# Optimization experiments

Measured on AMD Instinct MI355X. Metric: run time of the kernel, lower is better.

The kernel has to match this reference:

```python
import jax, jax.numpy as jnp
import numpy as np

DIM = 1024
NH = 16        # query heads
NKV = 4        # kv heads
HD = 64        # head dim
GROUPS = NH // NKV
SPATIAL = 16
NZ = SPATIAL * SPATIAL  # 256 latent tokens with 2D structure
SOFT_CAP = 50.0
SCALE = HD ** -0.5
EPS = 1e-6


def rope_2d_cos_sin(nz, hd, spatial, dtype):
    # 2D RoPE: first half of head_dim encodes row position, second half column.
    pos = jnp.arange(nz)
    row = (pos // spatial).astype(jnp.float32)
    col = (pos % spatial).astype(jnp.float32)
    quarter = hd // 4
    inv_freq = 1.0 / (10000.0 ** (jnp.arange(quarter, dtype=jnp.float32) / quarter))
    f_row = row[:, None] * inv_freq[None, :]   # (nz, hd/4)
    f_col = col[:, None] * inv_freq[None, :]   # (nz, hd/4)
    emb = jnp.concatenate([f_row, f_col], axis=-1)      # (nz, hd/2)
    emb = jnp.concatenate([emb, emb], axis=-1)          # (nz, hd)
    return jnp.cos(emb).astype(dtype), jnp.sin(emb).astype(dtype)


def rotate_half(x):
    x1, x2 = jnp.split(x, 2, axis=-1)
    return jnp.concatenate([-x2, x1], axis=-1)


def apply_rotary(x, cos, sin):
    return x * cos + rotate_half(x) * sin


def rms_norm(x, w):
    # RMSNorm over head_dim with learned per-dim scale (QKNorm)
    return x * jax.lax.rsqrt(jnp.mean(x * x, axis=-1, keepdims=True) + EPS) * w


def setup_inputs() -> dict:
    key = jax.random.key(0)
    ks = jax.random.split(key, 7)
    B, T, S = 4, 16, 264
    x = jax.random.normal(ks[0], (B, T, S, DIM), dtype=jnp.float32)
    wq = jax.random.normal(ks[1], (NH * HD, DIM), dtype=jnp.float32) * 0.02
    wk = jax.random.normal(ks[2], (NKV * HD, DIM), dtype=jnp.float32) * 0.02
    wv = jax.random.normal(ks[3], (NKV * HD, DIM), dtype=jnp.float32) * 0.02
    wo = jax.random.normal(ks[4], (DIM, NH * HD), dtype=jnp.float32) * 0.02
    q_norm_w = jnp.ones((HD,), dtype=jnp.float32)
    k_norm_w = jnp.ones((HD,), dtype=jnp.float32)
    return {"x": x, "wq": wq, "wk": wk, "wv": wv, "wo": wo,
            "q_norm_w": q_norm_w, "k_norm_w": k_norm_w}


def reference(x, wq, wk, wv, wo, q_norm_w, k_norm_w):
    B, T, S, D = x.shape
    xf = x.reshape(B * T, S, D)
    # projections (torch Linear: y = x @ W.T)
    q = (xf @ wq.T).reshape(B * T, S, NH, HD).transpose(0, 2, 1, 3)   # (BT,NH,S,HD)
    k = (xf @ wk.T).reshape(B * T, S, NKV, HD).transpose(0, 2, 1, 3)  # (BT,NKV,S,HD)
    v = (xf @ wv.T).reshape(B * T, S, NKV, HD).transpose(0, 2, 1, 3)
    # QKNorm
    q = rms_norm(q, q_norm_w)
    k = rms_norm(k, k_norm_w)
    # partial 2D RoPE on latent tokens only
    cos, sin = rope_2d_cos_sin(NZ, HD, SPATIAL, q.dtype)
    cos = cos[None, None]  # (1,1,NZ,HD)
    sin = sin[None, None]
    q = jnp.concatenate([apply_rotary(q[:, :, :NZ], cos, sin), q[:, :, NZ:]], axis=2)
    k = jnp.concatenate([apply_rotary(k[:, :, :NZ], cos, sin), k[:, :, NZ:]], axis=2)
    # GQA: expand kv heads (repeat_interleave == jnp.repeat)
    k = jnp.repeat(k, GROUPS, axis=1)
    v = jnp.repeat(v, GROUPS, axis=1)
    # attention with soft cap
    attn = jnp.einsum("bhqd,bhkd->bhqk", q, k) * SCALE
    attn = SOFT_CAP * jnp.tanh(attn / SOFT_CAP)
    attn = jax.nn.softmax(attn, axis=-1)
    out = jnp.einsum("bhqk,bhkd->bhqd", attn, v)
    out = out.transpose(0, 2, 1, 3).reshape(B * T, S, NH * HD)
    out = out @ wo.T
    return out.reshape(B, T, S, D)
```

## Files before the change

### kernel.cpp

```cpp
#include <hip/hip_runtime.h>

typedef __bf16 bf16;
typedef __bf16 bf16x8 __attribute__((ext_vector_type(8)));
typedef float  f32x4  __attribute__((ext_vector_type(4)));

#define DIM   1024
#define NH    16
#define NKV   4
#define HD    64
#define SLEN  264
#define BTOT  64
#define MROWS (BTOT * SLEN)
#define NQKV  1536
#define NZ    256
#define VPAD  288

__device__ __forceinline__ void gl_lds16(const bf16* g, bf16* l) {
    __builtin_amdgcn_global_load_lds((__attribute__((address_space(1))) void*)(g),
                                     (__attribute__((address_space(3))) void*)(l),
                                     16, 0, 0);
}

__global__ void cvt_f32_bf16(const float* __restrict__ src, bf16* __restrict__ dst, int n) {
    int i = (blockIdx.x * 256 + threadIdx.x) * 4;
    if (i < n) {
        float4 v = *(const float4*)(src + i);
        dst[i + 0] = (bf16)v.x; dst[i + 1] = (bf16)v.y;
        dst[i + 2] = (bf16)v.z; dst[i + 3] = (bf16)v.w;
    }
}

__global__ void cvt_wcat(const float* __restrict__ wq, const float* __restrict__ wk,
                         const float* __restrict__ wv, bf16* __restrict__ dst) {
    int i = (blockIdx.x * 256 + threadIdx.x) * 4;
    const float* src; int off;
    if (i < 1024 * 1024)      { src = wq; off = i; }
    else if (i < 1280 * 1024) { src = wk; off = i - 1024 * 1024; }
    else                      { src = wv; off = i - 1280 * 1024; }
    float4 v = *(const float4*)(src + off);
    dst[i + 0] = (bf16)v.x; dst[i + 1] = (bf16)v.y;
    dst[i + 2] = (bf16)v.z; dst[i + 3] = (bf16)v.w;
}

__global__ void rope_tab_kernel(float2* __restrict__ ctab) {
    int i = blockIdx.x * 256 + threadIdx.x;
    int s = i >> 5, d = i & 31;
    const float LN1 = 0.5756462732485115f;
    float pos = (d < 16) ? (float)(s >> 4) : (float)(s & 15);
    float ang = pos * expf(-(float)(d & 15) * LN1);
    float sn, cs; sincosf(ang, &sn, &cs);
    ctab[i] = make_float2(cs, sn);
}

__device__ __forceinline__ int xcd_swizzle(int orig, int nwg) {
    int q = nwg >> 3, r = nwg & 7;
    int xcd = orig & 7, lid = orig >> 3;
    return (xcd < r ? xcd * (q + 1) : r * (q + 1) + (xcd - r) * q) + lid;
}


#define GATE2  asm volatile("s_waitcnt vmcnt(2)" ::: "memory")
#define NOGATE do {} while (0)

#define STAGE(DST, G, H, KT) do {                                              \
    gl_lds16((G) + (size_t)((H) * 128 + rs0) * DIM + (KT) * 64 + cs0 * 8,      \
             (DST) + wid * 512);                                               \
    gl_lds16((G) + (size_t)((H) * 128 + 64 + rs0) * DIM + (KT) * 64 + cs0 * 8, \
             (DST) + 4096 + wid * 512);                                        \
} while (0)

#define PHASE(Ad, Bd, AA, KS, STAGE_STMT, GATE_STMT) do {                      \
    bf16x8 af_[4], bf_[4];                                                     \
    _Pragma("unroll")                                                          \
    for (int i_ = 0; i_ < 4; i_++) {                                           \
        af_[i_] = *(const bf16x8*)((Ad) + aRdBase + i_ * 1024 + xorv[KS]);     \
        bf_[i_] = *(const bf16x8*)((Bd) + bRdBase + i_ * 1024 + xorv[KS]);     \
    }                                                                          \
    STAGE_STMT;                                                                \
    GATE_STMT;                                                                 \
    __builtin_amdgcn_s_barrier();                                              \
    asm volatile("s_waitcnt lgkmcnt(0)" ::: "memory");                         \
    __builtin_amdgcn_sched_barrier(0);                                         \
    __builtin_amdgcn_s_setprio(1);                                             \
    _Pragma("unroll")                                                          \
    for (int i_ = 0; i_ < 4; i_++)                                             \
        _Pragma("unroll")                                                      \
        for (int n_ = 0; n_ < 4; n_++)                                         \
            acc[AA][i_][n_] = __builtin_amdgcn_mfma_f32_16x16x32_bf16(         \
                af_[i_], bf_[n_], acc[AA][i_][n_], 0, 0, 0);                   \
    __builtin_amdgcn_s_setprio(0);                                             \
    __builtin_amdgcn_s_barrier();                                              \
} while (0)

__device__ __forceinline__ void gemm256_core(const bf16* __restrict__ Ag,
                                             const bf16* __restrict__ Bg,
                                             f32x4 (&acc)[2][4][4]) {
    __shared__ __align__(16) bf16 A00[128 * 64], A01[128 * 64], A10[128 * 64], A11[128 * 64];
    __shared__ __align__(16) bf16 B00[128 * 64], B01[128 * 64], B10[128 * 64], B11[128 * 64];

    const int tid  = threadIdx.x;
    const int wid  = tid >> 6, lane = tid & 63;
    const int quad = lane >> 4, r16 = lane & 15;
    const int wm = wid & 1, wn = wid >> 1;

    const int rs0 = tid >> 3;
    const int cs0 = (tid & 7) ^ (rs0 & 7);

    const int aRdBase = (wm * 64 + r16) * 64;
    const int bRdBase = ((wn & 1) * 64 + r16) * 64;
    const int xorv[2] = { (quad ^ (r16 & 7)) * 8, ((4 + quad) ^ (r16 & 7)) * 8 };

    const bf16* Bd0 = (wn & 2) ? B01 : B00;
    const bf16* Bd1 = (wn & 2) ? B11 : B10;

    STAGE(A00, Ag, 0, 0);
    STAGE(A01, Ag, 1, 0);
    STAGE(B00, Bg, 0, 0);
    STAGE(B01, Bg, 1, 0);
    STAGE(A10, Ag, 0, 1);
    GATE2;
    __builtin_amdgcn_s_barrier();

#pragma unroll 1
    for (int it = 0; it < 8; ++it) {
        const int t1 = 2 * it + 1;
        int t2 = 2 * it + 2; if (t2 > 15) t2 = 15;
        int t3 = 2 * it + 3; if (t3 > 15) t3 = 15;
        PHASE(A00, Bd0, 0, 0, STAGE(A11, Ag, 1, t1), NOGATE);
        PHASE(A00, Bd0, 0, 1, STAGE(B10, Bg, 0, t1), NOGATE);
        PHASE(A01, Bd0, 1, 0, STAGE(B11, Bg, 1, t1), NOGATE);
        PHASE(A01, Bd0, 1, 1, STAGE(A00, Ag, 0, t2), GATE2);
        PHASE(A10, Bd1, 0, 0, STAGE(A01, Ag, 1, t2), NOGATE);
        PHASE(A10, Bd1, 0, 1, STAGE(B00, Bg, 0, t2), NOGATE);
        PHASE(A11, Bd1, 1, 0, STAGE(B01, Bg, 1, t2), NOGATE);
        PHASE(A11, Bd1, 1, 1, STAGE(A10, Ag, 0, t3), GATE2);
    }
}

__global__ __launch_bounds__(512) void gemm_qkv(const bf16* __restrict__ A,
                                                const bf16* __restrict__ Bw,
                                                bf16* __restrict__ out,
                                                const float* __restrict__ qw,
                                                const float* __restrict__ kw,
                                                const float2* __restrict__ ctab) {
    const int nwg = (MROWS / 256) * (NQKV / 256);
    int wg = xcd_swizzle(blockIdx.x, nwg);
    const int bm = wg / 6, bn = wg - bm * 6;

    f32x4 acc[2][4][4];
#pragma unroll
    for (int a = 0; a < 2; a++)
#pragma unroll
        for (int i = 0; i < 4; i++)
#pragma unroll
            for (int n = 0; n < 4; n++) acc[a][i][n] = (f32x4){0.f, 0.f, 0.f, 0.f};

    gemm256_core(A + (size_t)bm * 256 * DIM, Bw + (size_t)bn * 256 * DIM, acc);

    const int tid  = threadIdx.x;
    const int wid  = tid >> 6, lane = tid & 63;
    const int quad = lane >> 4, r16 = lane & 15;
    const int wm = wid & 1, wn = wid >> 1;
    const int colbase = bn * 256 + wn * 64;
    const int rowb    = bm * 256 + wm * 64;

    if (bn < 5) {
        const float* w = (bn < 4) ? qw : kw;
        float wreg[4];
#pragma unroll
        for (int n = 0; n < 4; n++) wreg[n] = w[n * 16 + r16];
#pragma unroll
        for (int a = 0; a < 2; a++)
#pragma unroll
            for (int i = 0; i < 4; i++)
#pragma unroll
                for (int r = 0; r < 4; r++) {
                    float ss = 0.f;
#pragma unroll
                    for (int n = 0; n < 4; n++) ss += acc[a][i][n][r] * acc[a][i][n][r];
                    ss += __shfl_xor(ss, 1, 64);
                    ss += __shfl_xor(ss, 2, 64);
                    ss += __shfl_xor(ss, 4, 64);
                    ss += __shfl_xor(ss, 8, 64);
                    float rms = rsqrtf(ss * (1.f / 64.f) + 1e-6f);
                    float xv[4];
#pragma unroll
                    for (int n = 0; n < 4; n++) xv[n] = acc[a][i][n][r] * rms * wreg[n];
                    int gm = rowb + a * 128 + i * 16 + quad * 4 + r;
                    int s = gm % SLEN;
                    if (s < NZ) {
                        float2 cs0 = ctab[s * 32 + r16];
                        float2 cs1 = ctab[s * 32 + 16 + r16];
                        float a0 = xv[0] * cs0.x - xv[2] * cs0.y;
                        float a2 = xv[2] * cs0.x + xv[0] * cs0.y;
                        float a1 = xv[1] * cs1.x - xv[3] * cs1.y;
                        float a3 = xv[3] * cs1.x + xv[1] * cs1.y;
                        xv[0] = a0; xv[1] = a1; xv[2] = a2; xv[3] = a3;
                    }
                    size_t rowoff = (size_t)gm * NQKV + colbase + r16;
#pragma unroll
                    for (int n = 0; n < 4; n++) out[rowoff + n * 16] = (bf16)xv[n];
                }
    } else {
#pragma unroll
        for (int a = 0; a < 2; a++)
#pragma unroll
            for (int i = 0; i < 4; i++)
#pragma unroll
                for (int r = 0; r < 4; r++) {
                    int gm = rowb + a * 128 + i * 16 + quad * 4 + r;
                    size_t rowoff = (size_t)gm * NQKV + colbase + r16;
#pragma unroll
                    for (int n = 0; n < 4; n++) out[rowoff + n * 16] = (bf16)acc[a][i][n][r];
                }
    }
}

#define GEMM_STAGE_PTRS(Mptr, tileRow, K, P)                                   \
    const bf16* P[4];                                                          \
    {                                                                          \
        _Pragma("unroll")                                                      \
        for (int k = 0; k < 4; k++) {                                          \
            int s = k * 256 + tid;                                             \
            int r = s >> 3, cp = s & 7;                                        \
            int c = cp ^ (r & 7);                                              \
            P[k] = (Mptr) + (size_t)((tileRow) + r) * (K) + c * 8;             \
        }                                                                      \
    }

__device__ __forceinline__ int swz(int row, int chunk) {
    return row * 64 + ((chunk ^ (row & 7)) * 8);
}

__global__ __launch_bounds__(256) void gemm_bt(const bf16* __restrict__ A,
                                               const bf16* __restrict__ Bw,
                                               float* __restrict__ Cout) {
    __shared__ __align__(16) bf16 As[128 * 64];
    __shared__ __align__(16) bf16 Bs[128 * 64];
    const int tid  = threadIdx.x;
    const int wid  = tid >> 6, lane = tid & 63;
    const int quad = lane >> 4, r16 = lane & 15;
    const int bid = blockIdx.x;
    const int g = bid / 32, rr = bid - g * 32;
    const int bm = g * 4 + (rr & 3), bn = rr >> 2;
    const int wm = wid & 1, wn = wid >> 1;

    GEMM_STAGE_PTRS(A,  bm * 128, DIM, Ap)
    GEMM_STAGE_PTRS(Bw, bn * 128, DIM, Bp)

    f32x4 acc[4][4];
#pragma unroll
    for (int i = 0; i < 4; i++)
#pragma unroll
        for (int j = 0; j < 4; j++) acc[i][j] = (f32x4){0.f, 0.f, 0.f, 0.f};

    for (int k0 = 0; k0 < DIM; k0 += 64) {
        __syncthreads();
#pragma unroll
        for (int k = 0; k < 4; k++) {
            gl_lds16(Ap[k] + k0, As + (k * 256 + wid * 64) * 8);
            gl_lds16(Bp[k] + k0, Bs + (k * 256 + wid * 64) * 8);
        }
        __syncthreads();
#pragma unroll
        for (int ks = 0; ks < 2; ks++) {
            bf16x8 a[4], b[4];
#pragma unroll
            for (int i = 0; i < 4; i++) {
                a[i] = *(const bf16x8*)&As[swz(wm * 64 + i * 16 + r16, ks * 4 + quad)];
                b[i] = *(const bf16x8*)&Bs[swz(wn * 64 + i * 16 + r16, ks * 4 + quad)];
            }
#pragma unroll
            for (int i = 0; i < 4; i++)
#pragma unroll
                for (int j = 0; j < 4; j++)
                    acc[i][j] = __builtin_amdgcn_mfma_f32_16x16x32_bf16(a[i], b[j], acc[i][j], 0, 0, 0);
        }
    }

#pragma unroll
    for (int i = 0; i < 4; i++)
#pragma unroll
        for (int j = 0; j < 4; j++)
#pragma unroll
            for (int r = 0; r < 4; r++) {
                int gm = bm * 128 + wm * 64 + i * 16 + quad * 4 + r;
                int gn = bn * 128 + wn * 64 + j * 16 + r16;
                Cout[(size_t)gm * DIM + gn] = acc[i][j][r];
            }
}

__global__ __launch_bounds__(256) void vtrans_kernel(const bf16* __restrict__ qkv,
                                                     bf16* __restrict__ vt) {
    __shared__ bf16 Ls[64 * 272];
    const int tid = threadIdx.x;
    const int b = blockIdx.x, bt = b >> 2, kv = b & 3;
    const int part = tid >> 5;
    const int rr   = tid & 31;
#pragma unroll
    for (int pass = 0; pass < 9; ++pass) {
        int row = pass * 32 + rr;
        if (row < SLEN) {
            bf16x8 v = *(const bf16x8*)(qkv + (size_t)(bt * SLEN + row) * NQKV + 1280 + kv * 64 + part * 8);
#pragma unroll
            for (int j = 0; j < 8; j++) Ls[(part * 8 + j) * 272 + row] = v[j];
        }
    }
    __syncthreads();
    const int d = tid >> 2, seg = tid & 3;
    size_t obase = ((size_t)b * 64 + d) * VPAD;
#pragma unroll
    for (int m = 0; m < 9; ++m) {
        int col = seg * 72 + m * 8;
        bf16x8 o;
#pragma unroll
        for (int j = 0; j < 8; j++) {
            int s = col + j;
            o[j] = (s < SLEN) ? Ls[d * 272 + s] : (bf16)0.f;
        }
        *(bf16x8*)(vt + obase + col) = o;
    }
}

__global__ __launch_bounds__(256) void attn_kernel(const bf16* __restrict__ qkv,
                                                   const bf16* __restrict__ vt,
                                                   bf16* __restrict__ aout) {
    const int PLD = 40;
    __shared__ __align__(16) bf16 Pb[4][2][16 * PLD];

    const int tid = threadIdx.x;
    const int wid = tid >> 6, lane = tid & 63;
    const int quad = lane >> 4, r16 = lane & 15;
    const int qp = blockIdx.x;
    const int kv = blockIdx.y, bt = blockIdx.z;
    const int h = kv * 4 + wid;

    bf16x8 qa[2][2];
#pragma unroll
    for (int qi = 0; qi < 2; qi++) {
        int q0 = qp * 32 + qi * 16 + r16;
        int qcl = q0 < SLEN ? q0 : SLEN - 1;
        const bf16* qb = qkv + (size_t)(bt * SLEN + qcl) * NQKV + h * HD + quad * 8;
        qa[qi][0] = *(const bf16x8*)qb;
        qa[qi][1] = *(const bf16x8*)(qb + 32);
    }

    f32x4 oacc[2][4];
    float lsum[2][4];
#pragma unroll
    for (int qi = 0; qi < 2; qi++)
#pragma unroll
        for (int i = 0; i < 4; i++) { oacc[qi][i] = (f32x4){0.f, 0.f, 0.f, 0.f}; lsum[qi][i] = 0.f; }

    const bf16* kbase = qkv + (size_t)bt * SLEN * NQKV + 1024 + kv * HD + quad * 8;
    const bf16* vbase = vt + (size_t)(bt * 4 + kv) * HD * VPAD;

    bf16x8 nk[2][2];
#pragma unroll
    for (int kt = 0; kt < 2; kt++) {
        int key = kt * 16 + r16;
        const bf16* kp = kbase + (size_t)key * NQKV;
        nk[kt][0] = *(const bf16x8*)kp;
        nk[kt][1] = *(const bf16x8*)(kp + 32);
    }

    for (int c = 0; c < 9; ++c) {
        bf16x8 ck[2][2];
#pragma unroll
        for (int kt = 0; kt < 2; kt++) { ck[kt][0] = nk[kt][0]; ck[kt][1] = nk[kt][1]; }
        if (c < 8) {
#pragma unroll
            for (int kt = 0; kt < 2; kt++) {
                int key = (c + 1) * 32 + kt * 16 + r16;
                int kc = key < SLEN ? key : SLEN - 1;
                const bf16* kp = kbase + (size_t)kc * NQKV;
                nk[kt][0] = *(const bf16x8*)kp;
                nk[kt][1] = *(const bf16x8*)(kp + 32);
            }
        }
        bf16x8 cv[4];
#pragma unroll
        for (int dt = 0; dt < 4; ++dt)
            cv[dt] = *(const bf16x8*)(vbase + (size_t)(dt * 16 + r16) * VPAD + c * 32 + quad * 8);

        f32x4 s[2][2];
#pragma unroll
        for (int qi = 0; qi < 2; qi++)
#pragma unroll
            for (int kt = 0; kt < 2; kt++) {
                f32x4 t = (f32x4){0.f, 0.f, 0.f, 0.f};
                t = __builtin_amdgcn_mfma_f32_16x16x32_bf16(qa[qi][0], ck[kt][0], t, 0, 0, 0);
                t = __builtin_amdgcn_mfma_f32_16x16x32_bf16(qa[qi][1], ck[kt][1], t, 0, 0, 0);
                s[qi][kt] = t;
            }

#pragma unroll
        for (int qi = 0; qi < 2; qi++) {
            bf16* Pw = &Pb[wid][qi][0];
#pragma unroll
            for (int kt = 0; kt < 2; kt++)
#pragma unroll
                for (int r = 0; r < 4; ++r) {
                    int key = c * 32 + kt * 16 + r16;
                    float sc = s[qi][kt][r];
                    float z = sc * 0.0025f;
                    float z2 = z * z;
                    float poly = fmaf(z2, fmaf(z2, 0.133333333f, -0.333333333f), 1.f);
                    float p = exp2f(sc * 0.18033688f * poly);
                    p = (key < SLEN) ? p : 0.f;
                    bf16 pb = (bf16)p;
                    lsum[qi][r] += (float)pb;
                    Pw[(quad * 4 + r) * PLD + kt * 16 + r16] = pb;
                }
            bf16x8 pa = *(const bf16x8*)&Pw[r16 * PLD + quad * 8];
#pragma unroll
            for (int dt = 0; dt < 4; ++dt)
                oacc[qi][dt] = __builtin_amdgcn_mfma_f32_16x16x32_bf16(pa, cv[dt], oacc[qi][dt], 0, 0, 0);
        }
    }

#pragma unroll
    for (int qi = 0; qi < 2; qi++)
#pragma unroll
        for (int r = 0; r < 4; ++r) {
            float l = lsum[qi][r];
            l += __shfl_xor(l, 1, 64);
            l += __shfl_xor(l, 2, 64);
            l += __shfl_xor(l, 4, 64);
            l += __shfl_xor(l, 8, 64);
            float inv = 1.f / l;
            int q = qp * 32 + qi * 16 + quad * 4 + r;
            if (q < SLEN) {
                size_t base = (size_t)(bt * SLEN + q) * (NH * HD) + h * HD;
#pragma unroll
                for (int dt = 0; dt < 4; ++dt)
                    aout[base + dt * 16 + r16] = (bf16)(oacc[qi][dt][r] * inv);
            }
        }
}

extern "C" void kernel_launch(void* const* d_in, const int* in_sizes, int n_in,
                              void* d_out, int out_size, void* d_ws, size_t ws_size,
                              hipStream_t stream) {
    const float* x   = (const float*)d_in[0];
    const float* wq  = (const float*)d_in[1];
    const float* wk  = (const float*)d_in[2];
    const float* wv  = (const float*)d_in[3];
    const float* wo  = (const float*)d_in[4];
    const float* qnw = (const float*)d_in[5];
    const float* knw = (const float*)d_in[6];

    bf16* xbf  = (bf16*)d_ws;
    bf16* wcat = xbf  + (size_t)MROWS * DIM;
    bf16* wobf = wcat + (size_t)NQKV * DIM;
    bf16* qkv  = wobf + (size_t)DIM * DIM;
    bf16* vt   = qkv  + (size_t)MROWS * NQKV;
    float2* ctab = (float2*)(vt + (size_t)BTOT * NKV * HD * VPAD);
    bf16* aout = xbf;

    rope_tab_kernel<<<32, 256, 0, stream>>>(ctab);
    cvt_f32_bf16<<<(MROWS * DIM) / 1024, 256, 0, stream>>>(x, xbf, MROWS * DIM);
    cvt_wcat<<<(NQKV * DIM) / 1024, 256, 0, stream>>>(wq, wk, wv, wcat);
    cvt_f32_bf16<<<(DIM * DIM) / 1024, 256, 0, stream>>>(wo, wobf, DIM * DIM);

    gemm_qkv<<<(MROWS / 256) * (NQKV / 256), 512, 0, stream>>>(xbf, wcat, qkv, qnw, knw, ctab);
    vtrans_kernel<<<BTOT * NKV, 256, 0, stream>>>(qkv, vt);
    attn_kernel<<<dim3(9, NKV, BTOT), 256, 0, stream>>>(qkv, vt, aout);
    gemm_bt<<<(MROWS / 128) * (DIM / 128), 256, 0, stream>>>(aout, wobf, (float*)d_out);
}
```

Before: 344.8 us.

## Rewrite attention with 32x32 MFMA and register-only P transpose; merge prep kernels

The attention kernel moves from 16x16x32 MFMA tiles to 32x32x16 MFMA. It computes S^T (keys x queries) so the probabilities can be packed to bf16 and rearranged with v_permlane32_swap entirely in registers. This removes the LDS round-trip and per-element bf16 stores of P, and the row sum becomes a single cross-half shuffle. Separately, the weight conversion, Wo conversion and RoPE table kernels are merged into one launch to save launch overhead. The risk is higher register pressure from the 32x32 accumulators, and the row sum now uses unrounded fp32 p instead of the bf16-rounded values fed to the MFMA.

```diff
diff --git a/kernel.cpp b/kernel.cpp
--- a/kernel.cpp
+++ b/kernel.cpp
@@ -3,6 +3,8 @@
 typedef __bf16 bf16;
 typedef __bf16 bf16x8 __attribute__((ext_vector_type(8)));
 typedef float  f32x4  __attribute__((ext_vector_type(4)));
+typedef float  f32x16 __attribute__((ext_vector_type(16)));
+typedef unsigned int u32;
 
 #define DIM   1024
 #define NH    16
@@ -30,26 +32,34 @@
     }
 }
 
-__global__ void cvt_wcat(const float* __restrict__ wq, const float* __restrict__ wk,
-                         const float* __restrict__ wv, bf16* __restrict__ dst) {
-    int i = (blockIdx.x * 256 + threadIdx.x) * 4;
-    const float* src; int off;
-    if (i < 1024 * 1024)      { src = wq; off = i; }
-    else if (i < 1280 * 1024) { src = wk; off = i - 1024 * 1024; }
-    else                      { src = wv; off = i - 1280 * 1024; }
-    float4 v = *(const float4*)(src + off);
-    dst[i + 0] = (bf16)v.x; dst[i + 1] = (bf16)v.y;
-    dst[i + 2] = (bf16)v.z; dst[i + 3] = (bf16)v.w;
-}
-
-__global__ void rope_tab_kernel(float2* __restrict__ ctab) {
-    int i = blockIdx.x * 256 + threadIdx.x;
-    int s = i >> 5, d = i & 31;
-    const float LN1 = 0.5756462732485115f;
-    float pos = (d < 16) ? (float)(s >> 4) : (float)(s & 15);
-    float ang = pos * expf(-(float)(d & 15) * LN1);
-    float sn, cs; sincosf(ang, &sn, &cs);
-    ctab[i] = make_float2(cs, sn);
+__global__ void prep_misc(const float* __restrict__ wq, const float* __restrict__ wk,
+                          const float* __restrict__ wv, const float* __restrict__ wo,
+                          bf16* __restrict__ wcat, bf16* __restrict__ wobf,
+                          float2* __restrict__ ctab) {
+    int b = blockIdx.x, tid = threadIdx.x;
+    if (b < 1536) {
+        int i = (b * 256 + tid) * 4;
+        const float* src; int off;
+        if (i < 1024 * 1024)      { src = wq; off = i; }
+        else if (i < 1280 * 1024) { src = wk; off = i - 1024 * 1024; }
+        else                      { src = wv; off = i - 1280 * 1024; }
+        float4 v = *(const float4*)(src + off);
+        wcat[i + 0] = (bf16)v.x; wcat[i + 1] = (bf16)v.y;
+        wcat[i + 2] = (bf16)v.z; wcat[i + 3] = (bf16)v.w;
+    } else if (b < 2560) {
+        int i = ((b - 1536) * 256 + tid) * 4;
+        float4 v = *(const float4*)(wo + i);
+        wobf[i + 0] = (bf16)v.x; wobf[i + 1] = (bf16)v.y;
+        wobf[i + 2] = (bf16)v.z; wobf[i + 3] = (bf16)v.w;
+    } else {
+        int i = (b - 2560) * 256 + tid;
+        int s = i >> 5, d = i & 31;
+        const float LN1 = 0.5756462732485115f;
+        float pos = (d < 16) ? (float)(s >> 4) : (float)(s & 15);
+        float ang = pos * expf(-(float)(d & 15) * LN1);
+        float sn, cs; sincosf(ang, &sn, &cs);
+        ctab[i] = make_float2(cs, sn);
+    }
 }
 
 __device__ __forceinline__ int xcd_swizzle(int orig, int nwg) {
@@ -325,118 +335,104 @@
 __global__ __launch_bounds__(256) void attn_kernel(const bf16* __restrict__ qkv,
                                                    const bf16* __restrict__ vt,
                                                    bf16* __restrict__ aout) {
-    const int PLD = 40;
-    __shared__ __align__(16) bf16 Pb[4][2][16 * PLD];
-
+    __shared__ float invL[4][32];
     const int tid = threadIdx.x;
     const int wid = tid >> 6, lane = tid & 63;
-    const int quad = lane >> 4, r16 = lane & 15;
+    const int l31 = lane & 31, hi = lane >> 5;
     const int qp = blockIdx.x;
     const int kv = blockIdx.y, bt = blockIdx.z;
     const int h = kv * 4 + wid;
 
-    bf16x8 qa[2][2];
-#pragma unroll
-    for (int qi = 0; qi < 2; qi++) {
-        int q0 = qp * 32 + qi * 16 + r16;
-        int qcl = q0 < SLEN ? q0 : SLEN - 1;
-        const bf16* qb = qkv + (size_t)(bt * SLEN + qcl) * NQKV + h * HD + quad * 8;
-        qa[qi][0] = *(const bf16x8*)qb;
-        qa[qi][1] = *(const bf16x8*)(qb + 32);
-    }
-
-    f32x4 oacc[2][4];
-    float lsum[2][4];
-#pragma unroll
-    for (int qi = 0; qi < 2; qi++)
-#pragma unroll
-        for (int i = 0; i < 4; i++) { oacc[qi][i] = (f32x4){0.f, 0.f, 0.f, 0.f}; lsum[qi][i] = 0.f; }
-
-    const bf16* kbase = qkv + (size_t)bt * SLEN * NQKV + 1024 + kv * HD + quad * 8;
+    int q0 = qp * 32 + l31;
+    int qcl = q0 < SLEN ? q0 : SLEN - 1;
+    const bf16* qbase = qkv + (size_t)(bt * SLEN + qcl) * NQKV + h * HD + hi * 8;
+    bf16x8 qb[4];
+#pragma unroll
+    for (int s = 0; s < 4; s++) qb[s] = *(const bf16x8*)(qbase + s * 16);
+
+    const bf16* kbase = qkv + (size_t)bt * SLEN * NQKV + 1024 + kv * HD + hi * 8;
     const bf16* vbase = vt + (size_t)(bt * 4 + kv) * HD * VPAD;
 
-    bf16x8 nk[2][2];
-#pragma unroll
-    for (int kt = 0; kt < 2; kt++) {
-        int key = kt * 16 + r16;
-        const bf16* kp = kbase + (size_t)key * NQKV;
-        nk[kt][0] = *(const bf16x8*)kp;
-        nk[kt][1] = *(const bf16x8*)(kp + 32);
-    }
+    bf16x8 nka[4];
+    {
+        const bf16* kp = kbase + (size_t)l31 * NQKV;
+#pragma unroll
+        for (int s = 0; s < 4; s++) nka[s] = *(const bf16x8*)(kp + s * 16);
+    }
+
+    f32x16 oacc[2];
+#pragma unroll
+    for (int r = 0; r < 16; r++) { oacc[0][r] = 0.f; oacc[1][r] = 0.f; }
+    float lsum = 0.f;
 
     for (int c = 0; c < 9; ++c) {
-        bf16x8 ck[2][2];
-#pragma unroll
-        for (int kt = 0; kt < 2; kt++) { ck[kt][0] = nk[kt][0]; ck[kt][1] = nk[kt][1]; }
+        bf16x8 ka[4];
+#pragma unroll
+        for (int s = 0; s < 4; s++) ka[s] = nka[s];
         if (c < 8) {
-#pragma unroll
-            for (int kt = 0; kt < 2; kt++) {
-                int key = (c + 1) * 32 + kt * 16 + r16;
-                int kc = key < SLEN ? key : SLEN - 1;
-                const bf16* kp = kbase + (size_t)kc * NQKV;
-                nk[kt][0] = *(const bf16x8*)kp;
-                nk[kt][1] = *(const bf16x8*)(kp + 32);
-            }
-        }
-        bf16x8 cv[4];
-#pragma unroll
-        for (int dt = 0; dt < 4; ++dt)
-            cv[dt] = *(const bf16x8*)(vbase + (size_t)(dt * 16 + r16) * VPAD + c * 32 + quad * 8);
-
-        f32x4 s[2][2];
-#pragma unroll
-        for (int qi = 0; qi < 2; qi++)
-#pragma unroll
-            for (int kt = 0; kt < 2; kt++) {
-                f32x4 t = (f32x4){0.f, 0.f, 0.f, 0.f};
-                t = __builtin_amdgcn_mfma_f32_16x16x32_bf16(qa[qi][0], ck[kt][0], t, 0, 0, 0);
-                t = __builtin_amdgcn_mfma_f32_16x16x32_bf16(qa[qi][1], ck[kt][1], t, 0, 0, 0);
-                s[qi][kt] = t;
-            }
-
-#pragma unroll
-        for (int qi = 0; qi < 2; qi++) {
-            bf16* Pw = &Pb[wid][qi][0];
-#pragma unroll
-            for (int kt = 0; kt < 2; kt++)
-#pragma unroll
-                for (int r = 0; r < 4; ++r) {
-                    int key = c * 32 + kt * 16 + r16;
-                    float sc = s[qi][kt][r];
-                    float z = sc * 0.0025f;
-                    float z2 = z * z;
-                    float poly = fmaf(z2, fmaf(z2, 0.133333333f, -0.333333333f), 1.f);
-                    float p = exp2f(sc * 0.18033688f * poly);
-                    p = (key < SLEN) ? p : 0.f;
-                    bf16 pb = (bf16)p;
-                    lsum[qi][r] += (float)pb;
-                    Pw[(quad * 4 + r) * PLD + kt * 16 + r16] = pb;
-                }
-            bf16x8 pa = *(const bf16x8*)&Pw[r16 * PLD + quad * 8];
-#pragma unroll
-            for (int dt = 0; dt < 4; ++dt)
-                oacc[qi][dt] = __builtin_amdgcn_mfma_f32_16x16x32_bf16(pa, cv[dt], oacc[qi][dt], 0, 0, 0);
-        }
-    }
-
-#pragma unroll
-    for (int qi = 0; qi < 2; qi++)
-#pragma unroll
-        for (int r = 0; r < 4; ++r) {
-            float l = lsum[qi][r];
-            l += __shfl_xor(l, 1, 64);
-            l += __shfl_xor(l, 2, 64);
-            l += __shfl_xor(l, 4, 64);
-            l += __shfl_xor(l, 8, 64);
-            float inv = 1.f / l;
-            int q = qp * 32 + qi * 16 + quad * 4 + r;
-            if (q < SLEN) {
-                size_t base = (size_t)(bt * SLEN + q) * (NH * HD) + h * HD;
-#pragma unroll
-                for (int dt = 0; dt < 4; ++dt)
-                    aout[base + dt * 16 + r16] = (bf16)(oacc[qi][dt][r] * inv);
-            }
-        }
+            int key = (c + 1) * 32 + l31;
+            int kc = key < SLEN ? key : SLEN - 1;
+            const bf16* kp = kbase + (size_t)kc * NQKV;
+#pragma unroll
+            for (int s = 0; s < 4; s++) nka[s] = *(const bf16x8*)(kp + s * 16);
+        }
+        bf16x8 vb[2][2];
+#pragma unroll
+        for (int dt = 0; dt < 2; dt++)
+#pragma unroll
+            for (int st = 0; st < 2; st++)
+                vb[dt][st] = *(const bf16x8*)(vbase + (size_t)(dt * 32 + l31) * VPAD + c * 32 + st * 16 + hi * 8);
+
+        f32x16 sacc;
+#pragma unroll
+        for (int r = 0; r < 16; r++) sacc[r] = 0.f;
+#pragma unroll
+        for (int s = 0; s < 4; s++)
+            sacc = __builtin_amdgcn_mfma_f32_32x32x16_bf16(ka[s], qb[s], sacc, 0, 0, 0);
+
+        float p[16];
+#pragma unroll
+        for (int r = 0; r < 16; ++r) {
+            int key = c * 32 + (r & 3) + 8 * (r >> 2) + 4 * hi;
+            float sc = sacc[r];
+            float z = sc * 0.0025f;
+            float z2 = z * z;
+            float poly = fmaf(z2, fmaf(z2, 0.133333333f, -0.333333333f), 1.f);
+            float pv = exp2f(sc * 0.18033688f * poly);
+            pv = (key < SLEN) ? pv : 0.f;
+            p[r] = pv;
+            lsum += pv;
+        }
+#pragma unroll
+        for (int st = 0; st < 2; st++) {
+            u32 wA, wB, wC, wD;
+            asm("v_cvt_pk_bf16_f32 %0, %1, %2" : "=v"(wA) : "v"(p[st*8+0]), "v"(p[st*8+1]));
+            asm("v_cvt_pk_bf16_f32 %0, %1, %2" : "=v"(wB) : "v"(p[st*8+2]), "v"(p[st*8+3]));
+            asm("v_cvt_pk_bf16_f32 %0, %1, %2" : "=v"(wC) : "v"(p[st*8+4]), "v"(p[st*8+5]));
+            asm("v_cvt_pk_bf16_f32 %0, %1, %2" : "=v"(wD) : "v"(p[st*8+6]), "v"(p[st*8+7]));
+            asm volatile("v_permlane32_swap_b32 %0, %1" : "+v"(wA), "+v"(wC));
+            asm volatile("v_permlane32_swap_b32 %0, %1" : "+v"(wB), "+v"(wD));
+            union { u32 u[4]; bf16x8 v; } pa;
+            pa.u[0] = wA; pa.u[1] = wB; pa.u[2] = wC; pa.u[3] = wD;
+#pragma unroll
+            for (int dt = 0; dt < 2; dt++)
+                oacc[dt] = __builtin_amdgcn_mfma_f32_32x32x16_bf16(pa.v, vb[dt][st], oacc[dt], 0, 0, 0);
+        }
+    }
+
+    lsum += __shfl_xor(lsum, 32, 64);
+    invL[wid][l31] = 1.f / lsum;
+#pragma unroll
+    for (int r = 0; r < 16; ++r) {
+        int qloc = (r & 3) + 8 * (r >> 2) + 4 * hi;
+        int q = qp * 32 + qloc;
+        if (q < SLEN) {
+            float inv = invL[wid][qloc];
+            size_t base = (size_t)(bt * SLEN + q) * (NH * HD) + h * HD + l31;
+            aout[base]      = (bf16)(oacc[0][r] * inv);
+            aout[base + 32] = (bf16)(oacc[1][r] * inv);
+        }
+    }
 }
 
 extern "C" void kernel_launch(void* const* d_in, const int* in_sizes, int n_in,
@@ -458,10 +454,8 @@
     float2* ctab = (float2*)(vt + (size_t)BTOT * NKV * HD * VPAD);
     bf16* aout = xbf;
 
-    rope_tab_kernel<<<32, 256, 0, stream>>>(ctab);
+    prep_misc<<<2592, 256, 0, stream>>>(wq, wk, wv, wo, wcat, wobf, ctab);
     cvt_f32_bf16<<<(MROWS * DIM) / 1024, 256, 0, stream>>>(x, xbf, MROWS * DIM);
-    cvt_wcat<<<(NQKV * DIM) / 1024, 256, 0, stream>>>(wq, wk, wv, wcat);
-    cvt_f32_bf16<<<(DIM * DIM) / 1024, 256, 0, stream>>>(wo, wobf, DIM * DIM);
 
     gemm_qkv<<<(MROWS / 256) * (NQKV / 256), 512, 0, stream>>>(xbf, wcat, qkv, qnw, knw, ctab);
     vtrans_kernel<<<BTOT * NKV, 256, 0, stream>>>(qkv, vt);
```

Result: no change. 338.6 us (-1.8%).
